# Kernel optimization log

Measured on AMD Instinct MI355X. Metric: run time of the kernel, lower is better.

The kernel has to match this reference:

```python
import jax, jax.numpy as jnp
import numpy as np

N_NODES = 20000
N_EDGES = 320000
HIDDEN = 64
HEADS = 8
HEAD_DIM = HIDDEN // HEADS
K_HOPS = 2
CST = 1e-05


def setup_inputs() -> dict:
    key = jax.random.key(0)
    ks = jax.random.split(key, 12)
    s = 1.0 / np.sqrt(HIDDEN)
    inp = {
        "x": jax.random.normal(ks[0], (N_NODES, HIDDEN), dtype=jnp.float32),
        "edge_index": jax.random.randint(ks[1], (2, N_EDGES), 0, N_NODES, dtype=jnp.int64),
        "edge_feature": jnp.zeros((1,), dtype=jnp.float32),  # unused by the module
        "Wq": jax.random.uniform(ks[2], (HIDDEN, HIDDEN), jnp.float32, -s, s),
        "bq": jax.random.uniform(ks[3], (HIDDEN,), jnp.float32, -s, s),
        "Wk": jax.random.uniform(ks[4], (HIDDEN, HIDDEN), jnp.float32, -s, s),
        "bk": jax.random.uniform(ks[5], (HIDDEN,), jnp.float32, -s, s),
        "Wv": jax.random.uniform(ks[6], (HIDDEN, HIDDEN), jnp.float32, -s, s),
        "bv": jax.random.uniform(ks[7], (HIDDEN,), jnp.float32, -s, s),
        "Wo": jax.random.uniform(ks[8], (HIDDEN, HIDDEN), jnp.float32, -s, s),
        "bo": jax.random.uniform(ks[9], (HIDDEN,), jnp.float32, -s, s),
        "hopwise": jnp.ones((K_HOPS + 1,), dtype=jnp.float32),
        "headwise": jnp.zeros((HEADS, K_HOPS), dtype=jnp.float32),
    }
    return inp


def reference(x, edge_index, edge_feature, Wq, bq, Wk, bk, Wv, bv, Wo, bo, hopwise, headwise):
    N = x.shape[0]
    row, col = edge_index[0], edge_index[1]

    # symmetric normalization: deg is in-degree of col
    deg = jax.ops.segment_sum(jnp.ones_like(col, dtype=x.dtype), col, num_segments=N)
    deg_inv = jnp.where(deg > 0, deg ** -0.5, 0.0)
    norm = deg_inv[row] * deg_inv[col]  # [E]

    Q = 1.0 + jax.nn.elu(x @ Wq + bq)
    K = 1.0 + jax.nn.elu(x @ Wk + bk)
    V = (x @ Wv + bv)
    Q = Q.reshape(N, HEADS, HEAD_DIM)
    K = K.reshape(N, HEADS, HEAD_DIM)
    V = V.reshape(N, HEADS, HEAD_DIM)

    M = jnp.einsum('nhi,nhj->nhij', K, V)  # [N,H,d,d]
    hidden = V * hopwise[0]
    layerwise = jax.nn.softmax(headwise, axis=0)  # softmax over heads (dim=-2)

    for hop in range(K_HOPS):
        # scatter-add propagation: out[i] = sum_{e: col[e]=i} norm[e] * state[row[e]]
        M = jax.ops.segment_sum(norm[:, None, None, None] * M[row], col, num_segments=N)
        K = jax.ops.segment_sum(norm[:, None, None] * K[row], col, num_segments=N)
        H = jnp.einsum('nhi,nhij->nhj', Q, M)
        C = jnp.einsum('nhi,nhi->nh', Q, K)[..., None] + CST
        H = H / C
        gamma = hopwise[hop + 1] * layerwise[:, hop][:, None]  # [H,1]
        hidden = hidden + gamma * H

    hidden = hidden.reshape(N, HEADS * HEAD_DIM)
    # dropout is identity in eval mode
    return hidden @ Wo + bo
```

## Files before the change

kernel.cpp:

```cpp
#include <hip/hip_runtime.h>
#include <hip/hip_bf16.h>

typedef __hip_bfloat16 bf16;
typedef __fp16 half2_t __attribute__((ext_vector_type(2)));
typedef float floatx2 __attribute__((ext_vector_type(2)));

#define N_NODES 20000
#define N_EDGES 320000
#define CSTF 1e-5f

#if defined(__has_builtin)
#if __has_builtin(__builtin_amdgcn_cvt_pk_fp8_f32) && __has_builtin(__builtin_amdgcn_cvt_pk_f32_fp8)
#define M1FP8 1
#endif
#if __has_builtin(__builtin_amdgcn_fdot2)
#define HAVE_FDOT2 1
#endif
#endif

#ifdef M1FP8
#define M1_STRIDE 128
#define M1_LANE   2
typedef uint2 m1vec;
#else
#define M1_STRIDE 256
#define M1_LANE   4
typedef uint4 m1vec;
#endif

__device__ __forceinline__ half2_t u2h(unsigned int u) {
    union { unsigned int u; half2_t h; } c; c.u = u; return c.h;
}
__device__ __forceinline__ unsigned int pkh(float a, float b) {
    union { __fp16 h[2]; unsigned int u; } c;
    c.h[0] = (__fp16)a; c.h[1] = (__fp16)b;
    return c.u;
}
__device__ __forceinline__ float fdot2(half2_t a, half2_t b, float c) {
#ifdef HAVE_FDOT2
    return __builtin_amdgcn_fdot2(a, b, c, false);
#else
    return fmaf((float)a.x, (float)b.x, fmaf((float)a.y, (float)b.y, c));
#endif
}
__device__ __forceinline__ int rdl(int v, int lane) { return __builtin_amdgcn_readlane(v, lane); }
__device__ __forceinline__ float ldf(const void* p, int i, bool bf) {
    return bf ? __bfloat162float(((const bf16*)p)[i]) : ((const float*)p)[i];
}
__device__ __forceinline__ bool wave_is_i64(const void* ei, int e) {
    unsigned int hi = ((const unsigned int*)ei)[2 * e + 1];
    return !__any(hi != 0);
}

struct Args {
    const void *x, *ei, *Wq, *bq, *Wk, *bk, *Wv, *bv, *Wo, *bo, *hopwise, *headwise;
    void* out;
    float* Q;
    _Float16 *K0h, *Vh, *K1h;
    unsigned int* M1h;
    int* bsrc;
    int *deg, *cnt;
};

__global__ __launch_bounds__(256) void k_p1(Args a) {
    const int t = threadIdx.x;
    const int e = blockIdx.x * 256 + t;
    bool i64 = wave_is_i64(a.ei, e);
    int r, c;
    if (i64) {
        r = (int)((const long long*)a.ei)[e];
        c = (int)((const long long*)a.ei)[N_EDGES + e];
    } else {
        r = ((const int*)a.ei)[e];
        c = ((const int*)a.ei)[N_EDGES + e];
    }
    int slot = atomicAdd(&a.deg[c], 1);
    if (slot < 64) a.bsrc[c * 64 + slot] = r;
    if (blockIdx.x < 64) {
        int bad = 0;
        for (int i = blockIdx.x * 256 + t; i < 40000; i += 64 * 256) {
            unsigned int w = ((const unsigned int*)a.x)[i];
            if (((w >> 7)  & 0xFFu) == 0xFFu) bad++;
            if (((w >> 23) & 0xFFu) == 0xFFu) bad++;
        }
        if (bad) atomicAdd(&a.cnt[0], bad);
    }
}

__global__ __launch_bounds__(256) void k_p2(Args a) {
    __shared__ __fp16 sWh[3 * 4096];
    __shared__ float sx[4][64];
    const int t = threadIdx.x;
    const bool bf = (a.cnt[0] < 16);
    for (int i = t; i < 4096; i += 256) {
        int k = i >> 6, col = i & 63;
        int di_ = (k >> 1) * 128 + col * 2 + (k & 1);
        sWh[di_]        = (__fp16)ldf(a.Wq, i, bf);
        sWh[4096 + di_] = (__fp16)ldf(a.Wk, i, bf);
        sWh[8192 + di_] = (__fp16)ldf(a.Wv, i, bf);
    }
    __syncthreads();
    const unsigned int* sWq = (const unsigned int*)sWh;
    const unsigned int* sWk = sWq + 2048;
    const unsigned int* sWv = sWq + 4096;
    const int l = t & 63, sub = t >> 6;
    const float bqv = ldf(a.bq, l, bf), bkv = ldf(a.bk, l, bf), bvv = ldf(a.bv, l, bf);
    const int n0 = blockIdx.x * 8;
    for (int g = 0; g < 2; g++) {
        int n = n0 + g * 4 + sub;
        __syncthreads();
        sx[sub][l] = ldf(a.x, n * 64 + l, bf);
        __syncthreads();
        float q = bqv, k = bkv, v = bvv;
        const float2* xp = (const float2*)sx[sub];
#pragma unroll 8
        for (int kp = 0; kp < 32; kp++) {
            float2 xv = xp[kp];
            half2_t xh = u2h(pkh(xv.x, xv.y));
            q = fdot2(xh, u2h(sWq[kp * 64 + l]), q);
            k = fdot2(xh, u2h(sWk[kp * 64 + l]), k);
            v = fdot2(xh, u2h(sWv[kp * 64 + l]), v);
        }
        int dg = a.deg[n];
        float di = dg > 0 ? rsqrtf((float)dg) : 0.0f;
        a.Q[n * 64 + l] = q > 0.0f ? q + 1.0f : __expf(q);
        float kel = k > 0.0f ? k + 1.0f : __expf(k);
        a.K0h[n * 64 + l] = (_Float16)(di * kel);
        a.Vh[n * 64 + l]  = (_Float16)v;
    }
}

__global__ __launch_bounds__(128) void k_hop1(Args a) {
    const int l = threadIdx.x & 63;
    const int n = blockIdx.x * 2 + (threadIdx.x >> 6);
    const int hb = l & 56;
    float acc[8] = {0, 0, 0, 0, 0, 0, 0, 0};
    float kacc = 0.0f;
    const int dg = a.deg[n];
    const int m = min(dg, 64);
    if (m > 0) {
        const int srcv = a.bsrc[n * 64 + (l < m ? l : m - 1)];
#define H1_BODY(KU, VO, KO)                                                \
    {                                                                      \
        half2_t p0 = u2h(KU.x), p1 = u2h(KU.y), p2 = u2h(KU.z), p3 = u2h(KU.w); \
        float vv = (float)VO;                                              \
        acc[0] = fmaf(vv, (float)p0.x, acc[0]); acc[1] = fmaf(vv, (float)p0.y, acc[1]); \
        acc[2] = fmaf(vv, (float)p1.x, acc[2]); acc[3] = fmaf(vv, (float)p1.y, acc[3]); \
        acc[4] = fmaf(vv, (float)p2.x, acc[4]); acc[5] = fmaf(vv, (float)p2.y, acc[5]); \
        acc[6] = fmaf(vv, (float)p3.x, acc[6]); acc[7] = fmaf(vv, (float)p3.y, acc[7]); \
        kacc += (float)KO;                                                 \
    }
        int e = 0;
        for (; e + 4 <= m; e += 4) {
            int sA = rdl(srcv, e), sB = rdl(srcv, e + 1), sC = rdl(srcv, e + 2), sD = rdl(srcv, e + 3);
            uint4 kA = *(const uint4*)(a.K0h + sA * 64 + hb);
            uint4 kB = *(const uint4*)(a.K0h + sB * 64 + hb);
            uint4 kC = *(const uint4*)(a.K0h + sC * 64 + hb);
            uint4 kD = *(const uint4*)(a.K0h + sD * 64 + hb);
            __fp16 vA = a.Vh[sA * 64 + l], vB = a.Vh[sB * 64 + l];
            __fp16 vC = a.Vh[sC * 64 + l], vD = a.Vh[sD * 64 + l];
            __fp16 oA = a.K0h[sA * 64 + l], oB = a.K0h[sB * 64 + l];
            __fp16 oC = a.K0h[sC * 64 + l], oD = a.K0h[sD * 64 + l];
            H1_BODY(kA, vA, oA)
            H1_BODY(kB, vB, oB)
            H1_BODY(kC, vC, oC)
            H1_BODY(kD, vD, oD)
        }
        for (; e < m; e++) {
            int sA = rdl(srcv, e);
            uint4 kA = *(const uint4*)(a.K0h + sA * 64 + hb);
            __fp16 vA = a.Vh[sA * 64 + l];
            __fp16 oA = a.K0h[sA * 64 + l];
            H1_BODY(kA, vA, oA)
        }
#undef H1_BODY
        float inv = 1.0f / (float)dg;
#pragma unroll
        for (int i = 0; i < 8; i++) acc[i] *= inv;
        kacc *= inv;
    }
#ifdef M1FP8
    unsigned int w0 = 0, w1 = 0;
    w0 = __builtin_amdgcn_cvt_pk_fp8_f32(acc[0], acc[1], w0, false);
    w0 = __builtin_amdgcn_cvt_pk_fp8_f32(acc[2], acc[3], w0, true);
    w1 = __builtin_amdgcn_cvt_pk_fp8_f32(acc[4], acc[5], w1, false);
    w1 = __builtin_amdgcn_cvt_pk_fp8_f32(acc[6], acc[7], w1, true);
    uint2 o2; o2.x = w0; o2.y = w1;
    *(uint2*)(a.M1h + (size_t)n * M1_STRIDE + l * M1_LANE) = o2;
#else
    uint4 o;
    o.x = pkh(acc[0], acc[1]); o.y = pkh(acc[2], acc[3]);
    o.z = pkh(acc[4], acc[5]); o.w = pkh(acc[6], acc[7]);
    *(uint4*)(a.M1h + (size_t)n * M1_STRIDE + l * M1_LANE) = o;
#endif
    a.K1h[n * 64 + l] = (_Float16)kacc;
}

__global__ __launch_bounds__(128) void k_hop2f(Args a) {
    const bool bf = (a.cnt[0] < 16);
    const int l = threadIdx.x & 63;
    const int n = blockIdx.x * 2 + (threadIdx.x >> 6);
    const int hb = l & 56, h = l >> 3;
    const float4 qa = *(const float4*)(a.Q + n * 64 + hb);
    const float4 qb = *(const float4*)(a.Q + n * 64 + hb + 4);
    const float qown = a.Q[n * 64 + l];
    float hacc = 0.0f, sk = 0.0f;
    const int dg = a.deg[n];
    const int m = min(dg, 64);
#ifdef M1FP8
#define H2_DOT(MU, DST)                                                    \
    {                                                                      \
        floatx2 a0 = __builtin_amdgcn_cvt_pk_f32_fp8(MU.x, false);         \
        floatx2 a1 = __builtin_amdgcn_cvt_pk_f32_fp8(MU.x, true);          \
        floatx2 a2 = __builtin_amdgcn_cvt_pk_f32_fp8(MU.y, false);         \
        floatx2 a3 = __builtin_amdgcn_cvt_pk_f32_fp8(MU.y, true);          \
        DST = qa.x * a0.x;                                                 \
        DST = fmaf(qa.y, a0.y, DST); DST = fmaf(qa.z, a1.x, DST);          \
        DST = fmaf(qa.w, a1.y, DST); DST = fmaf(qb.x, a2.x, DST);          \
        DST = fmaf(qb.y, a2.y, DST); DST = fmaf(qb.z, a3.x, DST);          \
        DST = fmaf(qb.w, a3.y, DST);                                       \
    }
#else
    const half2_t q01 = u2h(pkh(qa.x, qa.y));
    const half2_t q23 = u2h(pkh(qa.z, qa.w));
    const half2_t q45 = u2h(pkh(qb.x, qb.y));
    const half2_t q67 = u2h(pkh(qb.z, qb.w));
#define H2_DOT(MU, DST)                                                    \
    {                                                                      \
        DST = fdot2(q01, u2h(MU.x), 0.0f);                                 \
        DST = fdot2(q23, u2h(MU.y), DST);                                  \
        DST = fdot2(q45, u2h(MU.z), DST);                                  \
        DST = fdot2(q67, u2h(MU.w), DST);                                  \
    }
#endif
    if (m > 0) {
        const int srcv = a.bsrc[n * 64 + (l < m ? l : m - 1)];
        int e = 0;
        for (; e + 8 <= m; e += 8) {
            int s_[8];
            m1vec m_[8];
            __fp16 k_[8];
#pragma unroll
            for (int u = 0; u < 8; u++) s_[u] = rdl(srcv, e + u);
#pragma unroll
            for (int u = 0; u < 8; u++) m_[u] = *(const m1vec*)(a.M1h + (size_t)s_[u] * M1_STRIDE + l * M1_LANE);
#pragma unroll
            for (int u = 0; u < 8; u++) k_[u] = a.K1h[s_[u] * 64 + l];
#pragma unroll
            for (int u = 0; u < 8; u++) {
                float d;
                H2_DOT(m_[u], d)
                hacc += d;
                sk += (float)k_[u];
            }
        }
        for (; e < m; e++) {
            int sA = rdl(srcv, e);
            m1vec mA = *(const m1vec*)(a.M1h + (size_t)sA * M1_STRIDE + l * M1_LANE);
            __fp16 kA = a.K1h[sA * 64 + l];
            float d;
            H2_DOT(mA, d)
            hacc += d;
            sk += (float)kA;
        }
    }
    m1vec mo = *(const m1vec*)(a.M1h + (size_t)n * M1_STRIDE + l * M1_LANE);
    float h1r;
    H2_DOT(mo, h1r)
#undef H2_DOT
    const float din = dg > 0 ? rsqrtf((float)dg) : 0.0f;
    const float sq  = dg > 0 ? sqrtf((float)dg)  : 0.0f;
    float h1 = h1r * sq;
    float c1 = qown * (float)a.K1h[n * 64 + l];
    float c2 = qown * sk;
#pragma unroll
    for (int dd = 1; dd < 8; dd <<= 1) {
        c1 += __shfl_xor(c1, dd);
        c2 += __shfl_xor(c2, dd);
    }
    c1 *= sq;
    c2 *= din;
    float H2v = hacc * din;

    float hw0 = ldf(a.hopwise, 0, bf), hw1 = ldf(a.hopwise, 1, bf), hw2 = ldf(a.hopwise, 2, bf);
    float e0 = 0.0f, e1 = 0.0f;
#pragma unroll
    for (int hh = 0; hh < 8; hh++) {
        e0 += __expf(ldf(a.headwise, hh * 2 + 0, bf));
        e1 += __expf(ldf(a.headwise, hh * 2 + 1, bf));
    }
    float g1 = hw1 * __expf(ldf(a.headwise, h * 2 + 0, bf)) / e0;
    float g2 = hw2 * __expf(ldf(a.headwise, h * 2 + 1, bf)) / e1;

    float hidden = hw0 * (float)a.Vh[n * 64 + l] + g1 * h1 / (c1 + CSTF) + g2 * H2v / (c2 + CSTF);

    float o = ldf(a.bo, l, bf);
#pragma unroll 16
    for (int k = 0; k < 64; k++) {
        float hk = __shfl(hidden, k);
        o += hk * ldf(a.Wo, k * 64 + l, bf);
    }
    if (bf) ((bf16*)a.out)[n * 64 + l] = __float2bfloat16(o);
    else    ((float*)a.out)[n * 64 + l] = o;
}

extern "C" void kernel_launch(void* const* d_in, const int* in_sizes, int n_in,
                              void* d_out, int out_size, void* d_ws, size_t ws_size,
                              hipStream_t stream) {
    char* p = (char*)d_ws;
    auto alloc = [&](size_t bytes) {
        void* r = (void*)p;
        p += (bytes + 255) & ~(size_t)255;
        return r;
    };
    Args a;
    a.x = d_in[0];  a.ei = d_in[1];
    a.Wq = d_in[3]; a.bq = d_in[4];
    a.Wk = d_in[5]; a.bk = d_in[6];
    a.Wv = d_in[7]; a.bv = d_in[8];
    a.Wo = d_in[9]; a.bo = d_in[10];
    a.hopwise = d_in[11]; a.headwise = d_in[12];
    a.out = d_out;

    a.Q    = (float*)alloc((size_t)N_NODES * 64 * 4);
    a.K0h  = (_Float16*)alloc((size_t)N_NODES * 64 * 2);
    a.Vh   = (_Float16*)alloc((size_t)N_NODES * 64 * 2);
    a.K1h  = (_Float16*)alloc((size_t)N_NODES * 64 * 2);
    a.M1h  = (unsigned int*)alloc((size_t)N_NODES * 1024);
    a.bsrc = (int*)alloc((size_t)N_NODES * 64 * 4);
    int* zz = (int*)alloc(((size_t)N_NODES + 64) * 4);
    a.deg = zz;
    a.cnt = zz + N_NODES;

    (void)hipMemsetAsync(zz, 0, ((size_t)N_NODES + 64) * 4, stream);

    const int EB = (N_EDGES + 255) / 256;
    k_p1<<<EB, 256, 0, stream>>>(a);
    k_p2<<<2500, 256, 0, stream>>>(a);
    k_hop1<<<N_NODES / 2, 128, 0, stream>>>(a);
    k_hop2f<<<N_NODES / 2, 128, 0, stream>>>(a);
}
```

Before: 193.1 us.

## Use MFMA for QKV and output projections, split output GEMM into own kernel

Replaces the scalar fdot2-based QKV projection with a 64-node-per-block MFMA 16x16x32 f16 GEMM using swizzled LDS tiles. It also moves the Wo projection out of the hop2 kernel into a new MFMA kernel that reads an fp32 hidden buffer, and precomputes the hop/head gamma coefficients once. This removes per-node weight reloads and the 64-step shuffle loop. In exchange it adds a kernel launch and a global round trip of the hidden activations.

```diff
diff --git a/kernel.cpp b/kernel.cpp
--- a/kernel.cpp
+++ b/kernel.cpp
@@ -4,6 +4,8 @@
 typedef __hip_bfloat16 bf16;
 typedef __fp16 half2_t __attribute__((ext_vector_type(2)));
 typedef float floatx2 __attribute__((ext_vector_type(2)));
+typedef _Float16 f16x8_t __attribute__((ext_vector_type(8)));
+typedef float f32x4_t __attribute__((ext_vector_type(4)));
 
 #define N_NODES 20000
 #define N_EDGES 320000
@@ -59,6 +61,8 @@
     _Float16 *K0h, *Vh, *K1h;
     unsigned int* M1h;
     int* bsrc;
+    float* Hf;
+    float* gam;
     int *deg, *cnt;
 };
 
@@ -87,46 +91,89 @@
     }
 }
 
-__global__ __launch_bounds__(256) void k_p2(Args a) {
-    __shared__ __fp16 sWh[3 * 4096];
-    __shared__ float sx[4][64];
+__global__ __launch_bounds__(256) void k_qkv(Args a) {
+    __shared__ __align__(16) _Float16 sA[4096];
+    __shared__ __align__(16) _Float16 sB[12288];
     const int t = threadIdx.x;
     const bool bf = (a.cnt[0] < 16);
-    for (int i = t; i < 4096; i += 256) {
-        int k = i >> 6, col = i & 63;
-        int di_ = (k >> 1) * 128 + col * 2 + (k & 1);
-        sWh[di_]        = (__fp16)ldf(a.Wq, i, bf);
-        sWh[4096 + di_] = (__fp16)ldf(a.Wk, i, bf);
-        sWh[8192 + di_] = (__fp16)ldf(a.Wv, i, bf);
+    const int n0 = blockIdx.x * 64;
+
+    if (blockIdx.x == 0 && t < 8) {
+        float e0 = 0.f, e1 = 0.f;
+        for (int hh = 0; hh < 8; hh++) {
+            e0 += __expf(ldf(a.headwise, hh * 2 + 0, bf));
+            e1 += __expf(ldf(a.headwise, hh * 2 + 1, bf));
+        }
+        a.gam[t]     = ldf(a.hopwise, 1, bf) * __expf(ldf(a.headwise, t * 2 + 0, bf)) / e0;
+        a.gam[8 + t] = ldf(a.hopwise, 2, bf) * __expf(ldf(a.headwise, t * 2 + 1, bf)) / e1;
+        if (t == 0) a.gam[16] = ldf(a.hopwise, 0, bf);
+    }
+
+    for (int i = t; i < 2048; i += 256) {
+        int node = i >> 5, kp = i & 31;
+        int gn = n0 + node; if (gn >= N_NODES) gn = N_NODES - 1;
+        float x0 = ldf(a.x, gn * 64 + kp * 2 + 0, bf);
+        float x1 = ldf(a.x, gn * 64 + kp * 2 + 1, bf);
+        int byte = (node * 128 + kp * 4) ^ ((node & 7) << 4);
+        *(unsigned int*)((char*)sA + byte) = pkh(x0, x1);
+    }
+    for (int i = t; i < 6144; i += 256) {
+        int kp = i / 192, n = i % 192;
+        int k = kp * 2, c = n & 63;
+        const void* W = (n < 64) ? a.Wq : (n < 128) ? a.Wk : a.Wv;
+        float w0 = ldf(W, k * 64 + c, bf);
+        float w1 = ldf(W, (k + 1) * 64 + c, bf);
+        int ct = n >> 4, kh = k >> 5, kq = (k & 31) >> 3;
+        int hoff = (((ct * 2 + kh) * 64 + kq * 16 + (n & 15)) << 3) + (k & 7);
+        *(unsigned int*)&sB[hoff] = pkh(w0, w1);
     }
     __syncthreads();
-    const unsigned int* sWq = (const unsigned int*)sWh;
-    const unsigned int* sWk = sWq + 2048;
-    const unsigned int* sWv = sWq + 4096;
-    const int l = t & 63, sub = t >> 6;
-    const float bqv = ldf(a.bq, l, bf), bkv = ldf(a.bk, l, bf), bvv = ldf(a.bv, l, bf);
-    const int n0 = blockIdx.x * 8;
-    for (int g = 0; g < 2; g++) {
-        int n = n0 + g * 4 + sub;
-        __syncthreads();
-        sx[sub][l] = ldf(a.x, n * 64 + l, bf);
-        __syncthreads();
-        float q = bqv, k = bkv, v = bvv;
-        const float2* xp = (const float2*)sx[sub];
-#pragma unroll 8
-        for (int kp = 0; kp < 32; kp++) {
-            float2 xv = xp[kp];
-            half2_t xh = u2h(pkh(xv.x, xv.y));
-            q = fdot2(xh, u2h(sWq[kp * 64 + l]), q);
-            k = fdot2(xh, u2h(sWk[kp * 64 + l]), k);
-            v = fdot2(xh, u2h(sWv[kp * 64 + l]), v);
-        }
-        int dg = a.deg[n];
-        float di = dg > 0 ? rsqrtf((float)dg) : 0.0f;
-        a.Q[n * 64 + l] = q > 0.0f ? q + 1.0f : __expf(q);
-        float kel = k > 0.0f ? k + 1.0f : __expf(k);
-        a.K0h[n * 64 + l] = (_Float16)(di * kel);
-        a.Vh[n * 64 + l]  = (_Float16)v;
+
+    const int l = t & 63, w = t >> 6;
+    f16x8_t Afrag[2];
+    {
+        int node = w * 16 + (l & 15);
+        int cb = node * 128 + ((l >> 4) * 16);
+        int swz = (node & 7) << 4;
+        Afrag[0] = *(const f16x8_t*)((const char*)sA + ((cb)      ^ swz));
+        Afrag[1] = *(const f16x8_t*)((const char*)sA + ((cb + 64) ^ swz));
+    }
+    f32x4_t acc[12];
+#pragma unroll
+    for (int ct = 0; ct < 12; ct++) acc[ct] = (f32x4_t){0.f, 0.f, 0.f, 0.f};
+#pragma unroll
+    for (int kh = 0; kh < 2; kh++) {
+#pragma unroll
+        for (int ct = 0; ct < 12; ct++) {
+            f16x8_t B = *(const f16x8_t*)&sB[((ct * 2 + kh) * 64 + l) * 8];
+            acc[ct] = __builtin_amdgcn_mfma_f32_16x16x32_f16(Afrag[kh], B, acc[ct], 0, 0, 0);
+        }
+    }
+    const int dcol = l & 15;
+    float bqv[4], bkv[4], bvv[4];
+#pragma unroll
+    for (int ct = 0; ct < 4; ct++) {
+        bqv[ct] = ldf(a.bq, ct * 16 + dcol, bf);
+        bkv[ct] = ldf(a.bk, ct * 16 + dcol, bf);
+        bvv[ct] = ldf(a.bv, ct * 16 + dcol, bf);
+    }
+    const int rbase = n0 + w * 16 + ((l >> 4) << 2);
+#pragma unroll
+    for (int j = 0; j < 4; j++) {
+        int gn = rbase + j;
+        if (gn < N_NODES) {
+            int dg = a.deg[gn];
+            float di = dg > 0 ? rsqrtf((float)dg) : 0.0f;
+#pragma unroll
+            for (int ct = 0; ct < 4; ct++) {
+                float q = acc[ct][j] + bqv[ct];
+                a.Q[gn * 64 + ct * 16 + dcol] = q > 0.f ? q + 1.f : __expf(q);
+                float kx = acc[4 + ct][j] + bkv[ct];
+                float ke = kx > 0.f ? kx + 1.f : __expf(kx);
+                a.K0h[gn * 64 + ct * 16 + dcol] = (_Float16)(di * ke);
+                a.Vh[gn * 64 + ct * 16 + dcol] = (_Float16)(acc[8 + ct][j] + bvv[ct]);
+            }
+        }
     }
 }
 
@@ -197,7 +244,6 @@
 }
 
 __global__ __launch_bounds__(128) void k_hop2f(Args a) {
-    const bool bf = (a.cnt[0] < 16);
     const int l = threadIdx.x & 63;
     const int n = blockIdx.x * 2 + (threadIdx.x >> 6);
     const int hb = l & 56, h = l >> 3;
@@ -282,26 +328,72 @@
     c2 *= din;
     float H2v = hacc * din;
 
-    float hw0 = ldf(a.hopwise, 0, bf), hw1 = ldf(a.hopwise, 1, bf), hw2 = ldf(a.hopwise, 2, bf);
-    float e0 = 0.0f, e1 = 0.0f;
-#pragma unroll
-    for (int hh = 0; hh < 8; hh++) {
-        e0 += __expf(ldf(a.headwise, hh * 2 + 0, bf));
-        e1 += __expf(ldf(a.headwise, hh * 2 + 1, bf));
-    }
-    float g1 = hw1 * __expf(ldf(a.headwise, h * 2 + 0, bf)) / e0;
-    float g2 = hw2 * __expf(ldf(a.headwise, h * 2 + 1, bf)) / e1;
-
-    float hidden = hw0 * (float)a.Vh[n * 64 + l] + g1 * h1 / (c1 + CSTF) + g2 * H2v / (c2 + CSTF);
-
-    float o = ldf(a.bo, l, bf);
-#pragma unroll 16
-    for (int k = 0; k < 64; k++) {
-        float hk = __shfl(hidden, k);
-        o += hk * ldf(a.Wo, k * 64 + l, bf);
-    }
-    if (bf) ((bf16*)a.out)[n * 64 + l] = __float2bfloat16(o);
-    else    ((float*)a.out)[n * 64 + l] = o;
+    float hidden = a.gam[16] * (float)a.Vh[n * 64 + l]
+                 + a.gam[h] * h1 / (c1 + CSTF)
+                 + a.gam[8 + h] * H2v / (c2 + CSTF);
+    a.Hf[n * 64 + l] = hidden;
+}
+
+__global__ __launch_bounds__(256) void k_out(Args a) {
+    __shared__ __align__(16) _Float16 sA[4096];
+    __shared__ __align__(16) _Float16 sB[4096];
+    const int t = threadIdx.x;
+    const bool bf = (a.cnt[0] < 16);
+    const int n0 = blockIdx.x * 64;
+    for (int i = t; i < 2048; i += 256) {
+        int node = i >> 5, kp = i & 31;
+        int gn = n0 + node; if (gn >= N_NODES) gn = N_NODES - 1;
+        float2 hv = *(const float2*)(a.Hf + gn * 64 + kp * 2);
+        int byte = (node * 128 + kp * 4) ^ ((node & 7) << 4);
+        *(unsigned int*)((char*)sA + byte) = pkh(hv.x, hv.y);
+    }
+    for (int i = t; i < 2048; i += 256) {
+        int kp = i >> 6, c = i & 63;
+        int k = kp * 2;
+        float w0 = ldf(a.Wo, k * 64 + c, bf);
+        float w1 = ldf(a.Wo, (k + 1) * 64 + c, bf);
+        int ct = c >> 4, kh = k >> 5, kq = (k & 31) >> 3;
+        int hoff = (((ct * 2 + kh) * 64 + kq * 16 + (c & 15)) << 3) + (k & 7);
+        *(unsigned int*)&sB[hoff] = pkh(w0, w1);
+    }
+    __syncthreads();
+    const int l = t & 63, w = t >> 6;
+    f16x8_t Afrag[2];
+    {
+        int node = w * 16 + (l & 15);
+        int cb = node * 128 + ((l >> 4) * 16);
+        int swz = (node & 7) << 4;
+        Afrag[0] = *(const f16x8_t*)((const char*)sA + ((cb)      ^ swz));
+        Afrag[1] = *(const f16x8_t*)((const char*)sA + ((cb + 64) ^ swz));
+    }
+    f32x4_t acc[4];
+#pragma unroll
+    for (int ct = 0; ct < 4; ct++) acc[ct] = (f32x4_t){0.f, 0.f, 0.f, 0.f};
+#pragma unroll
+    for (int kh = 0; kh < 2; kh++) {
+#pragma unroll
+        for (int ct = 0; ct < 4; ct++) {
+            f16x8_t B = *(const f16x8_t*)&sB[((ct * 2 + kh) * 64 + l) * 8];
+            acc[ct] = __builtin_amdgcn_mfma_f32_16x16x32_f16(Afrag[kh], B, acc[ct], 0, 0, 0);
+        }
+    }
+    const int dcol = l & 15;
+    float bov[4];
+#pragma unroll
+    for (int ct = 0; ct < 4; ct++) bov[ct] = ldf(a.bo, ct * 16 + dcol, bf);
+    const int rbase = n0 + w * 16 + ((l >> 4) << 2);
+#pragma unroll
+    for (int j = 0; j < 4; j++) {
+        int gn = rbase + j;
+        if (gn < N_NODES) {
+#pragma unroll
+            for (int ct = 0; ct < 4; ct++) {
+                float o = acc[ct][j] + bov[ct];
+                if (bf) ((bf16*)a.out)[gn * 64 + ct * 16 + dcol] = __float2bfloat16(o);
+                else    ((float*)a.out)[gn * 64 + ct * 16 + dcol] = o;
+            }
+        }
+    }
 }
 
 extern "C" void kernel_launch(void* const* d_in, const int* in_sizes, int n_in,
@@ -327,7 +419,9 @@
     a.Vh   = (_Float16*)alloc((size_t)N_NODES * 64 * 2);
     a.K1h  = (_Float16*)alloc((size_t)N_NODES * 64 * 2);
     a.M1h  = (unsigned int*)alloc((size_t)N_NODES * 1024);
+    a.Hf   = (float*)alloc((size_t)N_NODES * 64 * 4);
     a.bsrc = (int*)alloc((size_t)N_NODES * 64 * 4);
+    a.gam  = (float*)alloc(256);
     int* zz = (int*)alloc(((size_t)N_NODES + 64) * 4);
     a.deg = zz;
     a.cnt = zz + N_NODES;
@@ -335,8 +429,10 @@
     (void)hipMemsetAsync(zz, 0, ((size_t)N_NODES + 64) * 4, stream);
 
     const int EB = (N_EDGES + 255) / 256;
+    const int GB = (N_NODES + 63) / 64;
     k_p1<<<EB, 256, 0, stream>>>(a);
-    k_p2<<<2500, 256, 0, stream>>>(a);
+    k_qkv<<<GB, 256, 0, stream>>>(a);
     k_hop1<<<N_NODES / 2, 128, 0, stream>>>(a);
     k_hop2f<<<N_NODES / 2, 128, 0, stream>>>(a);
-}
+    k_out<<<GB, 256, 0, stream>>>(a);
+}
```

Result: faster. 173.8 us (-10.0%).
